# Kernel optimization log

Hardware: AMD Instinct MI355X
Metric: run time of the kernel (lower is better)

The kernel has to match this reference:

```python
import jax, jax.numpy as jnp
import numpy as np

MODES = 32
WIDTH = 64


def crelu(z):
    # split-complex ReLU (torch.relu is undefined on complex; this is the standard fix)
    return jax.nn.relu(z.real) + 1j * jax.nn.relu(z.imag)


def _linear_params(key, fan_in, fan_out):
    k1, k2 = jax.random.split(key)
    s = 1.0 / np.sqrt(fan_in)
    W = jax.random.uniform(k1, (fan_out, fan_in), minval=-s, maxval=s, dtype=jnp.float32)
    b = jax.random.uniform(k2, (fan_out,), minval=-s, maxval=s, dtype=jnp.float32)
    return W, b


def setup_inputs() -> dict:
    key = jax.random.key(0)
    ks = jax.random.split(key, 8)
    B, G = 32768, 512
    H0, H1, H2 = 1024, 512, 64  # hidden_layers; H2 == WIDTH
    FD = 128                    # field_dim
    geometry_input = jax.random.normal(ks[0], (B, G), dtype=jnp.float32)
    W_in, b_in = _linear_params(ks[1], G, H0)
    W_h1, b_h1 = _linear_params(ks[2], H0, H1)
    W_h2, b_h2 = _linear_params(ks[3], H1, H2)
    w0 = jax.random.normal(ks[4], (MODES, WIDTH), dtype=jnp.float32)
    w1 = jax.random.normal(ks[5], (MODES, WIDTH), dtype=jnp.float32)
    lin1_W, lin1_b = _linear_params(ks[6], WIDTH, WIDTH)
    k7a, k7b = jax.random.split(ks[7])
    lin2_W, lin2_b = _linear_params(k7a, WIDTH, WIDTH)
    W_out, b_out = _linear_params(k7b, H2, FD)
    return dict(geometry_input=geometry_input, W_in=W_in, b_in=b_in,
                W_h1=W_h1, b_h1=b_h1, W_h2=W_h2, b_h2=b_h2,
                w0=w0, w1=w1, lin1_W=lin1_W, lin1_b=lin1_b,
                lin2_W=lin2_W, lin2_b=lin2_b, W_out=W_out, b_out=b_out)


def reference(geometry_input, W_in, b_in, W_h1, b_h1, W_h2, b_h2,
              w0, w1, lin1_W, lin1_b, lin2_W, lin2_b, W_out, b_out):
    # MLP encoder: [B, G] -> [B, 64]
    x = jax.nn.relu(geometry_input @ W_in.T + b_in)
    x = jax.nn.relu(x @ W_h1.T + b_h1)
    x = jax.nn.relu(x @ W_h2.T + b_h2)
    # FNO block
    xh = jnp.fft.fftn(x)  # fftn over ALL axes, as in torch code -> complex64 [B, 64]
    phase = jnp.exp(1j * 2.0 * jnp.pi * jnp.arange(MODES) / MODES).astype(jnp.complex64)
    y = xh[:, None, :] * w0  # per-mode lift: [B, MODES, WIDTH]
    y = crelu(y)
    y = y * phase[None, :, None]  # diagonal L mode-multiply
    y = jnp.einsum('bmw,mw->bw', y, w1.astype(y.dtype))  # collapse modes -> [B, WIDTH]
    y = crelu(y @ lin1_W.T + lin1_b)  # real weights on complex acts
    y = y @ lin2_W.T + lin2_b
    y = jnp.fft.ifftn(y)  # [B, 64] complex
    out = y @ W_out.T + b_out  # [B, field_dim] complex
    return out
```

## Files before the change

### kernel.cpp

```cpp
#include <hip/hip_runtime.h>
#include <hip/hip_bf16.h>


#define PI2F 6.28318530717958647692f

typedef __attribute__((ext_vector_type(8))) short short8;
typedef __attribute__((ext_vector_type(4))) float f32x4;

__device__ __forceinline__ unsigned short f2bf(float f) {
  unsigned int u = __float_as_uint(f);
  u += 0x7fff + ((u >> 16) & 1);
  return (unsigned short)(u >> 16);
}
__device__ __forceinline__ unsigned int pack_bf16x2(float a, float b) {
  return (unsigned int)f2bf(a) | ((unsigned int)f2bf(b) << 16);
}

__device__ __forceinline__ void gl2lds16(const void* gptr, const void* lptr) {
  __builtin_amdgcn_global_load_lds(
      (const __attribute__((address_space(1))) unsigned int*)(unsigned long long)gptr,
      (__attribute__((address_space(3))) unsigned int*)(unsigned int)(unsigned long long)lptr,
      16, 0, 0);
}

__global__ __launch_bounds__(256) void f32_to_bf16_k(
    const float* __restrict__ src, unsigned short* __restrict__ dst, int n4)
{
  int i = blockIdx.x * 256 + threadIdx.x;
  if (i < n4) {
    float4 v = ((const float4*)src)[i];
    uint2 p;
    p.x = pack_bf16x2(v.x, v.y);
    p.y = pack_bf16x2(v.z, v.w);
    ((uint2*)dst)[i] = p;
  }
}

template<int NBLOG, typename OUT>
__global__ __launch_bounds__(512, 1) void gemm_pipe(
    const unsigned short* __restrict__ A, const unsigned short* __restrict__ Bw,
    const float* __restrict__ bias, OUT* __restrict__ C, int N, int K)
{
  constexpr int BM = 128, BN = 256, BK = 64;
  constexpr int ASZ = BM * BK;
  constexpr int BSZ = BN * BK;
  constexpr int BUF = ASZ + BSZ;
  __shared__ __align__(16) unsigned short lds[3 * BUF];

  const int nwg = gridDim.x;
  const int cpx = nwg >> 3;
  const int orig = blockIdx.x;
  const int wg = (orig & 7) * cpx + (orig >> 3);
  const int mb = wg >> NBLOG;
  const int nb = wg & ((1 << NBLOG) - 1);
  const size_t m0 = (size_t)mb * BM;
  const size_t n0 = (size_t)nb * BN;

  const int tid = threadIdx.x;
  const int lane = tid & 63;
  const int wv = tid >> 6;
  const int q = lane >> 4, lr = lane & 15;
  const int x7 = lr & 7;
  const int wm = (wv >> 2) * 64;
  const int wn = (wv & 3) * 64;
  f32x4 acc[4][4] = {};

  auto STAGE_HALF = [&](int r, int kk, int s0) {
    unsigned short* dA = lds + r * BUF;
    #pragma unroll
    for (int u = 0; u < 3; ++u) {
      int e = wv * 6 + s0 + u;
      int isA = (e < 16) ? 1 : 0;
      int e2 = isA ? e : e - 16;
      int pc = e2 * 64 + lane;
      int row = pc >> 3, col = pc & 7;
      int lc = col ^ (row & 7);
      const unsigned short* src = isA ? A : Bw;
      size_t rb = isA ? m0 : n0;
      unsigned short* dst = dA + (isA ? 0 : ASZ) + e2 * 512;
      gl2lds16(src + (rb + row) * (size_t)K + kk + lc * 8, dst);
    }
  };

  const int nt = K / BK;
  STAGE_HALF(0, 0, 0); STAGE_HALF(0, 0, 3);
  STAGE_HALF(1, BK, 0); STAGE_HALF(1, BK, 3);
  asm volatile("s_waitcnt vmcnt(6)" ::: "memory");
  __builtin_amdgcn_s_barrier();

  int r0 = 0;
  for (int t = 0; t < nt; ++t) {
    const unsigned short* sA = lds + r0 * BUF;
    const unsigned short* sB = sA + ASZ;
    const bool st = (t + 2) < nt;
    const int r2 = (r0 >= 1) ? (r0 - 1) : 2;
    const int kk2 = (t + 2) * BK;

    short8 af[4][2], bf0[2][2];
    #pragma unroll
    for (int i = 0; i < 4; ++i)
      #pragma unroll
      for (int t2 = 0; t2 < 2; ++t2)
        af[i][t2] = *(const short8*)(sA + (wm + i * 16 + lr) * 64 + (((t2 << 2) | q) ^ x7) * 8);
    #pragma unroll
    for (int j = 0; j < 2; ++j)
      #pragma unroll
      for (int t2 = 0; t2 < 2; ++t2)
        bf0[j][t2] = *(const short8*)(sB + (wn + j * 16 + lr) * 64 + (((t2 << 2) | q) ^ x7) * 8);
    if (st) STAGE_HALF(r2, kk2, 0);
    __builtin_amdgcn_s_setprio(1);
    #pragma unroll
    for (int i = 0; i < 4; ++i)
      #pragma unroll
      for (int j = 0; j < 2; ++j)
        #pragma unroll
        for (int t2 = 0; t2 < 2; ++t2)
          acc[i][j] = __builtin_amdgcn_mfma_f32_16x16x32_bf16(af[i][t2], bf0[j][t2], acc[i][j], 0, 0, 0);
    __builtin_amdgcn_s_setprio(0);
    __builtin_amdgcn_s_barrier();

    short8 bf1[2][2];
    #pragma unroll
    for (int j = 0; j < 2; ++j)
      #pragma unroll
      for (int t2 = 0; t2 < 2; ++t2)
        bf1[j][t2] = *(const short8*)(sB + (wn + (j + 2) * 16 + lr) * 64 + (((t2 << 2) | q) ^ x7) * 8);
    if (st) STAGE_HALF(r2, kk2, 3);
    __builtin_amdgcn_s_setprio(1);
    #pragma unroll
    for (int i = 0; i < 4; ++i)
      #pragma unroll
      for (int j = 0; j < 2; ++j)
        #pragma unroll
        for (int t2 = 0; t2 < 2; ++t2)
          acc[i][j + 2] = __builtin_amdgcn_mfma_f32_16x16x32_bf16(af[i][t2], bf1[j][t2], acc[i][j + 2], 0, 0, 0);
    __builtin_amdgcn_s_setprio(0);

    asm volatile("s_waitcnt lgkmcnt(0)" ::: "memory");
    if (st) { asm volatile("s_waitcnt vmcnt(6)" ::: "memory"); }
    else    { asm volatile("s_waitcnt vmcnt(0)" ::: "memory"); }
    __builtin_amdgcn_s_barrier();
    r0 = (r0 + 1 >= 3) ? 0 : r0 + 1;
  }

  #pragma unroll
  for (int i = 0; i < 4; ++i)
    #pragma unroll
    for (int j = 0; j < 4; ++j) {
      size_t col = n0 + wn + j * 16 + lr;
      float bv = bias[col];
      #pragma unroll
      for (int r = 0; r < 4; ++r) {
        size_t row = m0 + wm + i * 16 + q * 4 + r;
        float v = acc[i][j][r] + bv;
        v = v > 0.f ? v : 0.f;
        if (sizeof(OUT) == 2) ((unsigned short*)C)[row * N + col] = f2bf(v);
        else                  ((float*)C)[row * N + col] = v;
      }
    }
}

template<int BM, int BN, int WM, int WN, typename OUT>
__global__ __launch_bounds__(256) void gemm_async(
    const unsigned short* __restrict__ A, const unsigned short* __restrict__ Bw,
    const float* __restrict__ bias, OUT* __restrict__ C,
    int M, int N, int K)
{
  constexpr int BK = 64;
  __shared__ __align__(16) unsigned short lA[BM * BK];
  __shared__ __align__(16) unsigned short lB[BN * BK];
  const int tid = threadIdx.x;
  const int lane = tid & 63;
  const int wv = tid >> 6;
  const int q = lane >> 4, lr = lane & 15;
  const int x7 = lr & 7;
  constexpr int WN_CNT = BN / WN;
  const int wm = (wv / WN_CNT) * WM;
  const int wn = (wv % WN_CNT) * WN;
  const size_t m0 = (size_t)blockIdx.x * BM;
  const size_t n0 = (size_t)blockIdx.y * BN;
  constexpr int MI = WM / 16, NI = WN / 16;
  f32x4 acc[MI][NI] = {};
  constexpr int A_INSTR = BM * BK / 512;
  constexpr int B_INSTR = BN * BK / 512;
  constexpr int A_PW = A_INSTR / 4, B_PW = B_INSTR / 4;
  (void)M;

  for (int k0 = 0; k0 < K; k0 += BK) {
    __syncthreads();
    #pragma unroll
    for (int s = 0; s < A_PW; ++s) {
      int instr = wv * A_PW + s;
      int pc = instr * 64 + lane;
      int row = pc >> 3, col = pc & 7;
      int lc = col ^ (row & 7);
      gl2lds16(A + (m0 + row) * K + k0 + lc * 8, lA + instr * 512);
    }
    #pragma unroll
    for (int s = 0; s < B_PW; ++s) {
      int instr = wv * B_PW + s;
      int pc = instr * 64 + lane;
      int row = pc >> 3, col = pc & 7;
      int lc = col ^ (row & 7);
      gl2lds16(Bw + (n0 + row) * K + k0 + lc * 8, lB + instr * 512);
    }
    __syncthreads();
    #pragma unroll
    for (int t = 0; t < 2; ++t) {
      short8 af[MI], bfr[NI];
      #pragma unroll
      for (int i = 0; i < MI; ++i) {
        int r = wm + i * 16 + lr;
        af[i] = *(const short8*)(lA + r * 64 + (((t << 2) | q) ^ x7) * 8);
      }
      #pragma unroll
      for (int j = 0; j < NI; ++j) {
        int r = wn + j * 16 + lr;
        bfr[j] = *(const short8*)(lB + r * 64 + (((t << 2) | q) ^ x7) * 8);
      }
      #pragma unroll
      for (int i = 0; i < MI; ++i)
        #pragma unroll
        for (int j = 0; j < NI; ++j)
          acc[i][j] = __builtin_amdgcn_mfma_f32_16x16x32_bf16(af[i], bfr[j], acc[i][j], 0, 0, 0);
    }
  }
  #pragma unroll
  for (int i = 0; i < MI; ++i)
    #pragma unroll
    for (int j = 0; j < NI; ++j) {
      size_t col = n0 + wn + j * 16 + lr;
      float bv = bias[col];
      #pragma unroll
      for (int r = 0; r < 4; ++r) {
        size_t row = m0 + wm + i * 16 + q * 4 + r;
        float v = acc[i][j][r] + bv;
        v = v > 0.f ? v : 0.f;
        if (sizeof(OUT) == 2) ((unsigned short*)C)[row * N + col] = f2bf(v);
        else                  ((float*)C)[row * N + col] = v;
      }
    }
}

__global__ __launch_bounds__(256) void precompute(
    const float* __restrict__ w0, const float* __restrict__ w1,
    const float* __restrict__ l2W, const float* __restrict__ l2b,
    float2* __restrict__ Ap, float2* __restrict__ Am,
    float2* __restrict__ Qt, float2* __restrict__ b2c)
{
  const int t = threadIdx.x;
  const int blk = blockIdx.x;
  if (blk == 0) {
    if (t < 64) {
      float apx = 0, apy = 0, amx = 0, amy = 0;
      for (int m = 0; m < 32; ++m) {
        float s0 = w0[m * 64 + t];
        float cf = w1[m * 64 + t] * s0;
        float sn, cs; sincosf(PI2F * (float)m / 32.f, &sn, &cs);
        if (s0 > 0.f)      { apx += cs * cf; apy += sn * cf; }
        else if (s0 < 0.f) { amx += cs * cf; amy += sn * cf; }
      }
      Ap[t] = make_float2(apx, apy);
      Am[t] = make_float2(amx, amy);
      float bx = 0, by = 0;
      for (int k = 0; k < 64; ++k) {
        float sn, cs; sincosf(PI2F * (float)((t * k) & 63) / 64.f, &sn, &cs);
        float lb = l2b[k] * (1.f / 64.f);
        bx += cs * lb; by += sn * lb;
      }
      b2c[t] = make_float2(bx, by);
    }
  } else {
    int e = (blk - 1) * 256 + t;
    int j = e >> 6, w = e & 63;
    float qx = 0, qy = 0;
    for (int k = 0; k < 64; ++k) {
      float sn, cs; sincosf(PI2F * (float)((j * k) & 63) / 64.f, &sn, &cs);
      float lw = l2W[k * 64 + w] * (1.f / 64.f);
      qx += cs * lw; qy += sn * lw;
    }
    Qt[w * 64 + j] = make_float2(qx, qy);
  }
}

__global__ __launch_bounds__(256) void dft64_rows(
    const float* __restrict__ x3, float2* __restrict__ xh1)
{
  __shared__ __align__(16) float xt[32][64];
  __shared__ float2 tw[64];
  const int t = threadIdx.x;
  const size_t b0 = (size_t)blockIdx.x * 32;
  for (int it = 0; it < 8; ++it) {
    int idx = it * 256 + t;
    int r = idx >> 6, w = idx & 63;
    xt[r][w] = x3[(b0 + r) * 64 + w];
  }
  if (t < 64) {
    float sn, cs; sincosf(-PI2F * (float)t / 64.f, &sn, &cs);
    tw[t] = make_float2(cs, sn);
  }
  __syncthreads();
  const int k = t & 63, rg = t >> 6;
  float2 acc[8] = {};
  #pragma unroll 1
  for (int w4 = 0; w4 < 16; ++w4) {
    int w = 4 * w4;
    int kw = k * w;
    float2 t0 = tw[kw & 63];
    float2 t1 = tw[(kw + k) & 63];
    float2 t2 = tw[(kw + 2 * k) & 63];
    float2 t3 = tw[(kw + 3 * k) & 63];
    #pragma unroll
    for (int r = 0; r < 8; ++r) {
      float4 xv = *(const float4*)(&xt[rg * 8 + r][w]);
      acc[r].x += xv.x * t0.x + xv.y * t1.x + xv.z * t2.x + xv.w * t3.x;
      acc[r].y += xv.x * t0.y + xv.y * t1.y + xv.z * t2.y + xv.w * t3.y;
    }
  }
  #pragma unroll
  for (int r = 0; r < 8; ++r)
    xh1[(b0 + rg * 8 + r) * 64 + k] = acc[r];
}

template<int SIGN>
__global__ __launch_bounds__(256) void fft_stage1(
    const float2* __restrict__ Xin, float2* __restrict__ T)
{
  __shared__ __align__(16) float2 tile[128 * 34];
  __shared__ float2 tw16s[16];
  const int blk = blockIdx.x;
  const int b2 = blk >> 1, wh = (blk & 1) * 32;
  const int t = threadIdx.x;
  #pragma unroll
  for (int it = 0; it < 8; ++it) {
    int idx = it * 256 + t;
    int b1 = idx >> 4, wi = (idx & 15) * 2;
    float4 v = *(const float4*)&Xin[((size_t)(b1 * 256 + b2)) * 64 + wh + wi];
    *(float4*)&tile[b1 * 34 + wi] = v;
  }
  if (t < 16) {
    float sn, cs; sincosf(SIGN * PI2F * (float)t / 16.f, &sn, &cs);
    tw16s[t] = make_float2(cs, sn);
  }
  __syncthreads();
  float2 twr[16];
  #pragma unroll
  for (int j = 0; j < 16; ++j) twr[j] = tw16s[j];

  {
    const int n2a = t >> 5, w = t & 31;
    float2 d[16];
    #pragma unroll
    for (int n1 = 0; n1 < 16; ++n1)
      d[n1] = tile[(8 * n1 + n2a) * 34 + w];
    float2 y[16];
    #pragma unroll
    for (int k = 0; k < 16; ++k) {
      float2 a = d[0];
      #pragma unroll
      for (int n1 = 1; n1 < 16; ++n1) {
        float2 tv = twr[(n1 * k) & 15];
        a.x += d[n1].x * tv.x - d[n1].y * tv.y;
        a.y += d[n1].x * tv.y + d[n1].y * tv.x;
      }
      y[k] = a;
    }
    float sstep, cstep;
    sincosf(SIGN * PI2F * (float)n2a / 128.f, &sstep, &cstep);
    float2 rot = make_float2(1.f, 0.f);
    #pragma unroll
    for (int k = 0; k < 16; ++k) {
      float2 a = y[k];
      y[k] = make_float2(a.x * rot.x - a.y * rot.y, a.x * rot.y + a.y * rot.x);
      float nrx = rot.x * cstep - rot.y * sstep;
      rot.y = rot.x * sstep + rot.y * cstep;
      rot.x = nrx;
    }
    __syncthreads();
    #pragma unroll
    for (int k = 0; k < 16; ++k)
      tile[(n2a * 16 + k) * 34 + w] = y[k];
  }
  __syncthreads();

  const int wB = t & 31, qB = t >> 5;
  float sstep, cstep;
  sincosf(SIGN * PI2F * (float)(16 * b2) / 32768.f, &sstep, &cstep);
  #pragma unroll
  for (int h = 0; h < 2; ++h) {
    const int k1p = qB + 8 * h;
    float2 d[8];
    #pragma unroll
    for (int n2 = 0; n2 < 8; ++n2)
      d[n2] = tile[(n2 * 16 + k1p) * 34 + wB];
    float2 acc[8];
    #pragma unroll
    for (int k2p = 0; k2p < 8; ++k2p) {
      float2 a = d[0];
      #pragma unroll
      for (int n2 = 1; n2 < 8; ++n2) {
        float2 tv = twr[(2 * n2 * k2p) & 15];
        a.x += d[n2].x * tv.x - d[n2].y * tv.y;
        a.y += d[n2].x * tv.y + d[n2].y * tv.x;
      }
      acc[k2p] = a;
    }
    float sb, cb;
    sincosf(SIGN * PI2F * (float)(b2 * k1p) / 32768.f, &sb, &cb);
    float2 rot = make_float2(cb, sb);
    #pragma unroll
    for (int k2p = 0; k2p < 8; ++k2p) {
      int k1 = k1p + 16 * k2p;
      float2 a = acc[k2p];
      T[((size_t)k1 * 256 + b2) * 64 + wh + wB] =
          make_float2(a.x * rot.x - a.y * rot.y, a.x * rot.y + a.y * rot.x);
      float nrx = rot.x * cstep - rot.y * sstep;
      rot.y = rot.x * sstep + rot.y * cstep;
      rot.x = nrx;
    }
  }
}

template<int SIGN, bool SCALE>
__global__ __launch_bounds__(256) void fft_stage2(
    const float2* __restrict__ T, float2* __restrict__ X)
{
  __shared__ __align__(16) float2 tile[256 * 18];
  __shared__ float2 tw16s[16];
  const int blk = blockIdx.x;
  const int k1 = blk >> 2, wq = (blk & 3) * 16;
  const int t = threadIdx.x;
  #pragma unroll
  for (int it = 0; it < 8; ++it) {
    int idx = it * 256 + t;
    int r2 = idx >> 3, wi = (idx & 7) * 2;
    float4 v = *(const float4*)&T[((size_t)k1 * 256 + r2) * 64 + wq + wi];
    *(float4*)&tile[r2 * 18 + wi] = v;
  }
  if (t < 16) {
    float sn, cs; sincosf(SIGN * PI2F * (float)t / 16.f, &sn, &cs);
    tw16s[t] = make_float2(cs, sn);
  }
  __syncthreads();
  float2 twr[16];
  #pragma unroll
  for (int j = 0; j < 16; ++j) twr[j] = tw16s[j];

  {
    const int n2a = t >> 4, w = t & 15;
    float2 d[16];
    #pragma unroll
    for (int n1 = 0; n1 < 16; ++n1)
      d[n1] = tile[(16 * n1 + n2a) * 18 + w];
    float2 y[16];
    #pragma unroll
    for (int k = 0; k < 16; ++k) {
      float2 a = d[0];
      #pragma unroll
      for (int n1 = 1; n1 < 16; ++n1) {
        float2 tv = twr[(n1 * k) & 15];
        a.x += d[n1].x * tv.x - d[n1].y * tv.y;
        a.y += d[n1].x * tv.y + d[n1].y * tv.x;
      }
      y[k] = a;
    }
    float sstep, cstep;
    sincosf(SIGN * PI2F * (float)n2a / 256.f, &sstep, &cstep);
    float2 rot = make_float2(1.f, 0.f);
    #pragma unroll
    for (int k = 0; k < 16; ++k) {
      float2 a = y[k];
      y[k] = make_float2(a.x * rot.x - a.y * rot.y, a.x * rot.y + a.y * rot.x);
      float nrx = rot.x * cstep - rot.y * sstep;
      rot.y = rot.x * sstep + rot.y * cstep;
      rot.x = nrx;
    }
    __syncthreads();
    #pragma unroll
    for (int k = 0; k < 16; ++k)
      tile[(n2a * 16 + k) * 18 + w] = y[k];
  }
  __syncthreads();

  const int k1pb = t >> 4, wB = t & 15;
  float2 d[16];
  #pragma unroll
  for (int n2 = 0; n2 < 16; ++n2)
    d[n2] = tile[(n2 * 16 + k1pb) * 18 + wB];
  const float sc = SCALE ? (1.f / 32768.f) : 1.f;
  #pragma unroll
  for (int k2p = 0; k2p < 16; ++k2p) {
    float2 a = d[0];
    #pragma unroll
    for (int n2 = 1; n2 < 16; ++n2) {
      float2 tv = twr[(n2 * k2p) & 15];
      a.x += d[n2].x * tv.x - d[n2].y * tv.y;
      a.y += d[n2].x * tv.y + d[n2].y * tv.x;
    }
    int k2 = k1pb + 16 * k2p;
    size_t row = (size_t)(k1 + 128 * k2);
    X[row * 64 + wq + wB] = make_float2(a.x * sc, a.y * sc);
  }
}

__global__ __launch_bounds__(256) void pw_lin(
    const float2* __restrict__ xh,
    const float2* __restrict__ Ap, const float2* __restrict__ Am,
    const float* __restrict__ l1W, const float* __restrict__ l1b,
    const float2* __restrict__ Qt, const float2* __restrict__ b2c,
    float2* __restrict__ u)
{
  __shared__ __align__(16) float2 tile[32][64];
  __shared__ __align__(16) float2 qt[64 * 64];
  const int t = threadIdx.x;
  const int lane = t & 63;
  const int wv = t >> 6;
  const size_t b0 = (size_t)blockIdx.x * 32;

  #pragma unroll
  for (int s = 0; s < 8; ++s) {
    int instr = wv * 8 + s;
    gl2lds16((const char*)Qt + instr * 1024 + lane * 16,
             (const char*)qt + instr * 1024);
  }

  for (int it = 0; it < 8; ++it) {
    int idx = it * 256 + t;
    int r = idx >> 6, w = idx & 63;
    float2 xv = xh[(b0 + r) * 64 + w];
    float2 Aa = (xv.x >= 0.f) ? Ap[w] : Am[w];
    float2 Ab = (xv.y >= 0.f) ? Ap[w] : Am[w];
    tile[r][w] = make_float2(xv.x * Aa.x - xv.y * Ab.y,
                             xv.x * Aa.y + xv.y * Ab.x);
  }
  __syncthreads();

  const int n = lane, rg = wv;

  {
    float2 acc[8] = {};
    const float* wrow = l1W + n * 64;
    float4 lwn = *(const float4*)wrow;
    #pragma unroll 1
    for (int w2 = 0; w2 < 16; ++w2) {
      float4 lw = lwn;
      lwn = *(const float4*)(wrow + 4 * ((w2 + 1) & 15));
      int w = 4 * w2;
      #pragma unroll
      for (int r = 0; r < 8; ++r) {
        const float4* rowp = (const float4*)(&tile[rg * 8 + r][w]);
        float4 y01 = rowp[0];
        float4 y23 = rowp[1];
        acc[r].x += y01.x * lw.x + y01.z * lw.y + y23.x * lw.z + y23.z * lw.w;
        acc[r].y += y01.y * lw.x + y01.w * lw.y + y23.y * lw.z + y23.w * lw.w;
      }
    }
    float bb = l1b[n];
    #pragma unroll
    for (int r = 0; r < 8; ++r) {
      float zr = acc[r].x + bb; zr = zr > 0.f ? zr : 0.f;
      float zi = acc[r].y;      zi = zi > 0.f ? zi : 0.f;
      tile[rg * 8 + r][n] = make_float2(zr, zi);
    }
  }

  {
    const int j = lane;
    float2 acc[8] = {};
    #pragma unroll 1
    for (int w2 = 0; w2 < 16; ++w2) {
      int w = 4 * w2;
      float2 q0 = qt[(w + 0) * 64 + j];
      float2 q1 = qt[(w + 1) * 64 + j];
      float2 q2 = qt[(w + 2) * 64 + j];
      float2 q3 = qt[(w + 3) * 64 + j];
      #pragma unroll
      for (int r = 0; r < 8; ++r) {
        const float4* rowp = (const float4*)(&tile[rg * 8 + r][w]);
        float4 z01 = rowp[0];
        float4 z23 = rowp[1];
        acc[r].x += z01.x * q0.x - z01.y * q0.y
                  + z01.z * q1.x - z01.w * q1.y
                  + z23.x * q2.x - z23.y * q2.y
                  + z23.z * q3.x - z23.w * q3.y;
        acc[r].y += z01.x * q0.y + z01.y * q0.x
                  + z01.z * q1.y + z01.w * q1.x
                  + z23.x * q2.y + z23.y * q2.x
                  + z23.z * q3.y + z23.w * q3.x;
      }
    }
    float2 bc = b2c[j];
    #pragma unroll
    for (int r = 0; r < 8; ++r)
      u[(b0 + rg * 8 + r) * 64 + j] = make_float2(acc[r].x + bc.x, acc[r].y + bc.y);
  }
}

template<int MODE>
__global__ __launch_bounds__(256) void final_out(
    const float2* __restrict__ v, const float* __restrict__ Wout,
    const float* __restrict__ bout, float* __restrict__ out)
{
  __shared__ __align__(16) float2 vt[32][64];
  const int t = threadIdx.x;
  const size_t b0 = (size_t)blockIdx.x * 32;
  for (int it = 0; it < 8; ++it) {
    int idx = it * 256 + t;
    int r = idx >> 6, w = idx & 63;
    vt[r][w] = v[(b0 + r) * 64 + w];
  }
  __syncthreads();
  const int f = t & 127, rg = t >> 7;
  const float* wrow = Wout + f * 64;
  float2 acc[16] = {};
  float2 wvn = *(const float2*)wrow;
  #pragma unroll 1
  for (int j2 = 0; j2 < 32; ++j2) {
    float2 wc = wvn;
    wvn = *(const float2*)(wrow + 2 * ((j2 + 1) & 31));
    #pragma unroll
    for (int r = 0; r < 16; ++r) {
      float4 vv = *(const float4*)(&vt[rg * 16 + r][2 * j2]);
      acc[r].x += vv.x * wc.x + vv.z * wc.y;
      acc[r].y += vv.y * wc.x + vv.w * wc.y;
    }
  }
  float bb = bout[f];
  #pragma unroll
  for (int r = 0; r < 16; ++r) {
    size_t idx = (b0 + rg * 16 + r) * 128 + f;
    if (MODE == 0) out[idx] = acc[r].x + bb;
    else ((float2*)out)[idx] = make_float2(acc[r].x + bb, acc[r].y);
  }
}

extern "C" void kernel_launch(void* const* d_in, const int* in_sizes, int n_in,
                              void* d_out, int out_size, void* d_ws, size_t ws_size,
                              hipStream_t stream)
{
  (void)in_sizes; (void)n_in; (void)ws_size;
  const float* geom = (const float*)d_in[0];
  const float* Win  = (const float*)d_in[1];
  const float* bin  = (const float*)d_in[2];
  const float* Wh1  = (const float*)d_in[3];
  const float* bh1  = (const float*)d_in[4];
  const float* Wh2  = (const float*)d_in[5];
  const float* bh2  = (const float*)d_in[6];
  const float* w0   = (const float*)d_in[7];
  const float* w1   = (const float*)d_in[8];
  const float* l1W  = (const float*)d_in[9];
  const float* l1b  = (const float*)d_in[10];
  const float* l2W  = (const float*)d_in[11];
  const float* l2b  = (const float*)d_in[12];
  const float* Wout = (const float*)d_in[13];
  const float* bout = (const float*)d_in[14];

  char* ws = (char*)d_ws;
  const size_t MB = 1048576ull;
  unsigned short* geomb = (unsigned short*)(ws);
  unsigned short* x2b   = (unsigned short*)(ws);
  unsigned short* x1b   = (unsigned short*)(ws + 32 * MB);
  float*  x3  = (float*)(ws + 32 * MB);
  float2* S0  = (float2*)(ws + 40 * MB);
  float2* S1  = (float2*)(ws + 56 * MB);
  float2* Ap  = (float2*)(ws + 72 * MB);
  float2* Am  = (float2*)(ws + 72 * MB + 512);
  float2* b2c = (float2*)(ws + 72 * MB + 1024);
  float2* Qt  = (float2*)(ws + 72 * MB + 1536);
  unsigned short* Winb = (unsigned short*)(ws + 96 * MB);
  unsigned short* Wh1b = (unsigned short*)(ws + 97 * MB);
  unsigned short* Wh2b = (unsigned short*)(ws + 98 * MB);

  f32_to_bf16_k<<<16384, 256, 0, stream>>>(geom, geomb, 4194304);
  f32_to_bf16_k<<<512, 256, 0, stream>>>(Win, Winb, 131072);
  f32_to_bf16_k<<<512, 256, 0, stream>>>(Wh1, Wh1b, 131072);
  f32_to_bf16_k<<<32, 256, 0, stream>>>(Wh2, Wh2b, 8192);

  gemm_pipe<2, unsigned short><<<1024, 512, 0, stream>>>(
      geomb, Winb, bin, x1b, 1024, 512);
  gemm_pipe<1, unsigned short><<<512, 512, 0, stream>>>(
      x1b, Wh1b, bh1, x2b, 512, 1024);
  gemm_async<128, 64,64,32,float><<<dim3(256, 1), 256, 0, stream>>>(
      x2b, Wh2b, bh2, x3, 32768, 64, 512);

  precompute<<<17, 256, 0, stream>>>(w0, w1, l2W, l2b, Ap, Am, Qt, b2c);
  dft64_rows<<<1024, 256, 0, stream>>>(x3, S0);
  fft_stage1<-1><<<512, 256, 0, stream>>>(S0, S1);
  fft_stage2<-1, false><<<512, 256, 0, stream>>>(S1, S0);
  pw_lin<<<1024, 256, 0, stream>>>(S0, Ap, Am, l1W, l1b, Qt, b2c, S1);
  fft_stage1<1><<<512, 256, 0, stream>>>(S1, S0);
  fft_stage2<1, true><<<512, 256, 0, stream>>>(S0, S1);
  if (out_size >= 8388608) {
    final_out<1><<<1024, 256, 0, stream>>>(S1, Wout, bout, (float*)d_out);
  } else {
    final_out<0><<<1024, 256, 0, stream>>>(S1, Wout, bout, (float*)d_out);
  }
}
```

Baseline: 414.9 us.

## Merge bf16 conversion launches and collapse GEMM main loop into one phase

Four separate f32-to-bf16 conversion launches are merged into a single kernel that dispatches on the global index, removing three launches. Separately, the pipelined GEMM's split half-iteration (two B-fragment loads, two staging halves, a mid-iteration barrier) becomes a single phase that loads all B fragments, stages the full next tile, and runs all MFMAs. This drops one barrier per K-step but raises register pressure and gives less interleaving of global loads with MFMA work.

After: 422.7 us. About the same (+1.9%).

```diff
diff --git a/kernel.cpp b/kernel.cpp
--- a/kernel.cpp
+++ b/kernel.cpp
@@ -23,17 +23,24 @@
       16, 0, 0);
 }
 
-__global__ __launch_bounds__(256) void f32_to_bf16_k(
-    const float* __restrict__ src, unsigned short* __restrict__ dst, int n4)
+__global__ __launch_bounds__(256) void conv_all(
+    const float* __restrict__ geom, const float* __restrict__ Win,
+    const float* __restrict__ Wh1, const float* __restrict__ Wh2,
+    unsigned short* __restrict__ dg, unsigned short* __restrict__ dw,
+    unsigned short* __restrict__ d1, unsigned short* __restrict__ d2)
 {
   int i = blockIdx.x * 256 + threadIdx.x;
-  if (i < n4) {
-    float4 v = ((const float4*)src)[i];
-    uint2 p;
-    p.x = pack_bf16x2(v.x, v.y);
-    p.y = pack_bf16x2(v.z, v.w);
-    ((uint2*)dst)[i] = p;
-  }
+  const float* s; unsigned short* d; int off;
+  if (i < 4194304)      { s = geom; d = dg; off = i; }
+  else if (i < 4325376) { s = Win;  d = dw; off = i - 4194304; }
+  else if (i < 4456448) { s = Wh1;  d = d1; off = i - 4325376; }
+  else if (i < 4464640) { s = Wh2;  d = d2; off = i - 4456448; }
+  else return;
+  float4 v = ((const float4*)s)[off];
+  uint2 p;
+  p.x = pack_bf16x2(v.x, v.y);
+  p.y = pack_bf16x2(v.z, v.w);
+  ((uint2*)d)[off] = p;
 }
 
 template<int NBLOG, typename OUT>
@@ -65,11 +72,11 @@
   const int wn = (wv & 3) * 64;
   f32x4 acc[4][4] = {};
 
-  auto STAGE_HALF = [&](int r, int kk, int s0) {
+  auto STAGE = [&](int r, int kk) {
     unsigned short* dA = lds + r * BUF;
     #pragma unroll
-    for (int u = 0; u < 3; ++u) {
-      int e = wv * 6 + s0 + u;
+    for (int u = 0; u < 6; ++u) {
+      int e = wv * 6 + u;
       int isA = (e < 16) ? 1 : 0;
       int e2 = isA ? e : e - 16;
       int pc = e2 * 64 + lane;
@@ -83,8 +90,8 @@
   };
 
   const int nt = K / BK;
-  STAGE_HALF(0, 0, 0); STAGE_HALF(0, 0, 3);
-  STAGE_HALF(1, BK, 0); STAGE_HALF(1, BK, 3);
+  STAGE(0, 0);
+  STAGE(1, BK);
   asm volatile("s_waitcnt vmcnt(6)" ::: "memory");
   __builtin_amdgcn_s_barrier();
 
@@ -96,44 +103,26 @@
     const int r2 = (r0 >= 1) ? (r0 - 1) : 2;
     const int kk2 = (t + 2) * BK;
 
-    short8 af[4][2], bf0[2][2];
+    short8 af[4][2], bfr[4][2];
     #pragma unroll
     for (int i = 0; i < 4; ++i)
       #pragma unroll
       for (int t2 = 0; t2 < 2; ++t2)
         af[i][t2] = *(const short8*)(sA + (wm + i * 16 + lr) * 64 + (((t2 << 2) | q) ^ x7) * 8);
     #pragma unroll
-    for (int j = 0; j < 2; ++j)
+    for (int j = 0; j < 4; ++j)
       #pragma unroll
       for (int t2 = 0; t2 < 2; ++t2)
-        bf0[j][t2] = *(const short8*)(sB + (wn + j * 16 + lr) * 64 + (((t2 << 2) | q) ^ x7) * 8);
-    if (st) STAGE_HALF(r2, kk2, 0);
+        bfr[j][t2] = *(const short8*)(sB + (wn + j * 16 + lr) * 64 + (((t2 << 2) | q) ^ x7) * 8);
+    if (st) STAGE(r2, kk2);
     __builtin_amdgcn_s_setprio(1);
     #pragma unroll
     for (int i = 0; i < 4; ++i)
       #pragma unroll
-      for (int j = 0; j < 2; ++j)
+      for (int j = 0; j < 4; ++j)
         #pragma unroll
         for (int t2 = 0; t2 < 2; ++t2)
-          acc[i][j] = __builtin_amdgcn_mfma_f32_16x16x32_bf16(af[i][t2], bf0[j][t2], acc[i][j], 0, 0, 0);
-    __builtin_amdgcn_s_setprio(0);
-    __builtin_amdgcn_s_barrier();
-
-    short8 bf1[2][2];
-    #pragma unroll
-    for (int j = 0; j < 2; ++j)
-      #pragma unroll
-      for (int t2 = 0; t2 < 2; ++t2)
-        bf1[j][t2] = *(const short8*)(sB + (wn + (j + 2) * 16 + lr) * 64 + (((t2 << 2) | q) ^ x7) * 8);
-    if (st) STAGE_HALF(r2, kk2, 3);
-    __builtin_amdgcn_s_setprio(1);
-    #pragma unroll
-    for (int i = 0; i < 4; ++i)
-      #pragma unroll
-      for (int j = 0; j < 2; ++j)
-        #pragma unroll
-        for (int t2 = 0; t2 < 2; ++t2)
-          acc[i][j + 2] = __builtin_amdgcn_mfma_f32_16x16x32_bf16(af[i][t2], bf1[j][t2], acc[i][j + 2], 0, 0, 0);
+          acc[i][j] = __builtin_amdgcn_mfma_f32_16x16x32_bf16(af[i][t2], bfr[j][t2], acc[i][j], 0, 0, 0);
     __builtin_amdgcn_s_setprio(0);
 
     asm volatile("s_waitcnt lgkmcnt(0)" ::: "memory");
@@ -671,10 +660,8 @@
   unsigned short* Wh1b = (unsigned short*)(ws + 97 * MB);
   unsigned short* Wh2b = (unsigned short*)(ws + 98 * MB);
 
-  f32_to_bf16_k<<<16384, 256, 0, stream>>>(geom, geomb, 4194304);
-  f32_to_bf16_k<<<512, 256, 0, stream>>>(Win, Winb, 131072);
-  f32_to_bf16_k<<<512, 256, 0, stream>>>(Wh1, Wh1b, 131072);
-  f32_to_bf16_k<<<32, 256, 0, stream>>>(Wh2, Wh2b, 8192);
+  conv_all<<<17441, 256, 0, stream>>>(geom, Win, Wh1, Wh2,
+                                      geomb, Winb, Wh1b, Wh2b);
 
   gemm_pipe<2, unsigned short><<<1024, 512, 0, stream>>>(
       geomb, Winb, bin, x1b, 1024, 512);
```
